# Performance work log

Measured on AMD Instinct MI355X. Metric: run time of the kernel, lower is better.

Reference implementation:

```python
import jax, jax.numpy as jnp
import numpy as np

N_USERS = 20000
N_ENTITIES = 80000
N = N_USERS + N_ENTITIES
EMBED_DIM = 128
CONV = [128, 128, 64, 32]  # [embed_dim] + eval(conv_dim_list)
NNZ = 1_600_000
CF_B = 8192
CF_L2_LAMBDA = 1e-5


def setup_inputs() -> dict:
    key = jax.random.key(0)
    ks = jax.random.split(key, 20)
    inp = {}
    inp["embed_table"] = jax.random.normal(ks[0], (N, EMBED_DIM), jnp.float32) * 0.02
    ki = 1
    for l in range(3):
        din, dout = CONV[l], CONV[l + 1]
        s = 1.0 / np.sqrt(din).astype(np.float32)
        inp[f"W1_{l}"] = jax.random.normal(ks[ki], (din, dout), jnp.float32) * s; ki += 1
        inp[f"b1_{l}"] = jnp.zeros((dout,), jnp.float32)
        inp[f"W2_{l}"] = jax.random.normal(ks[ki], (din, dout), jnp.float32) * s; ki += 1
        inp[f"b2_{l}"] = jnp.zeros((dout,), jnp.float32)
    inp["edge_rows"] = jax.random.randint(ks[7], (NNZ,), 0, N, jnp.int32)
    inp["edge_cols"] = jax.random.randint(ks[8], (NNZ,), 0, N, jnp.int32)
    # Laplacian-like normalized attention values (positive, ~1/degree scale)
    inp["edge_vals"] = jax.random.uniform(ks[9], (NNZ,), jnp.float32) / 16.0
    inp["user_ids"] = jax.random.randint(ks[10], (CF_B,), 0, N_USERS, jnp.int32)
    inp["item_pos_ids"] = jax.random.randint(ks[11], (CF_B,), N_USERS, N, jnp.int32)
    inp["item_neg_ids"] = jax.random.randint(ks[12], (CF_B,), N_USERS, N, jnp.int32)
    return inp


def _l2_normalize(x):
    # F.normalize(x, p=2, dim=1): x / max(||x||_2, eps)
    n = jnp.linalg.norm(x, axis=1, keepdims=True)
    return x / jnp.maximum(n, 1e-12)


def _l2_loss_mean(x):
    return jnp.mean(jnp.sum(x * x, axis=1) / 2.0)


def _calc_cf_embeddings(embed_table, layer_params, edge_rows, edge_cols, edge_vals):
    n = embed_table.shape[0]
    ego = embed_table
    outs = [ego]
    for (W1, b1, W2, b2) in layer_params:
        # sparse A @ ego via gather + segment_sum (SpMM in COO form)
        msgs = edge_vals[:, None] * ego[edge_cols]          # [nnz, d_in]
        side = jax.ops.segment_sum(msgs, edge_rows, num_segments=n)  # [n, d_in]
        # bi-interaction aggregator (mess_dropout = 0)
        ego = (jax.nn.leaky_relu((ego + side) @ W1 + b1)
               + jax.nn.leaky_relu((ego * side) @ W2 + b2))
        outs.append(_l2_normalize(ego))
    return jnp.concatenate(outs, axis=1)  # [n, 128+128+64+32]


def reference(embed_table, W1_0, b1_0, W2_0, b2_0, W1_1, b1_1, W2_1, b2_1,
              W1_2, b1_2, W2_2, b2_2, edge_rows, edge_cols, edge_vals,
              user_ids, item_pos_ids, item_neg_ids):
    layer_params = [(W1_0, b1_0, W2_0, b2_0),
                    (W1_1, b1_1, W2_1, b2_1),
                    (W1_2, b1_2, W2_2, b2_2)]
    all_embed = _calc_cf_embeddings(embed_table, layer_params,
                                    edge_rows, edge_cols, edge_vals)
    u = all_embed[user_ids]
    p = all_embed[item_pos_ids]
    ng = all_embed[item_neg_ids]
    pos_score = jnp.sum(u * p, axis=1)
    neg_score = jnp.sum(u * ng, axis=1)
    cf_loss = jnp.mean(-jax.nn.log_sigmoid(pos_score - neg_score))
    l2 = _l2_loss_mean(u) + _l2_loss_mean(p) + _l2_loss_mean(ng)
    return cf_loss + CF_L2_LAMBDA * l2
```

## Files before the change

### kernel.cpp

```cpp
#include <hip/hip_runtime.h>
#include <math.h>

static constexpr int N_NODES = 100000;
static constexpr int NNZ     = 1600000;
static constexpr int CFB     = 8192;
static constexpr int NBUCK   = (N_NODES + 63) / 64;
static constexpr int N4      = N_NODES * 128 / 4;
static constexpr int NCHUNK  = 128;
static constexpr int EPC     = NNZ / NCHUNK;
static constexpr int NE      = NBUCK * NCHUNK;
static constexpr int NBLK2   = (NE + 255) / 256;

typedef short bf16x8 __attribute__((ext_vector_type(8)));
typedef float f32x4  __attribute__((ext_vector_type(4)));

__device__ __forceinline__ float lrelu(float x) { return x >= 0.0f ? x : 0.01f * x; }

__device__ __forceinline__ unsigned short f2bf(float x) {
  unsigned u = __float_as_uint(x);
  u += 0x7FFFu + ((u >> 16) & 1u);
  return (unsigned short)(u >> 16);
}
__device__ __forceinline__ float bf2f(unsigned short h) {
  return __uint_as_float(((unsigned)h) << 16);
}
__device__ __forceinline__ unsigned pack2(float x, float y) {
  return (unsigned)f2bf(x) | ((unsigned)f2bf(y) << 16);
}

__global__ __launch_bounds__(256)
void cvt_bf16_kernel(const float* __restrict__ in, unsigned short* __restrict__ out) {
  int i = blockIdx.x * 256 + threadIdx.x;
  if (i < N4) {
    float4 v = reinterpret_cast<const float4*>(in)[i];
    uint2 o; o.x = pack2(v.x, v.y); o.y = pack2(v.z, v.w);
    reinterpret_cast<uint2*>(out)[i] = o;
  }
}

__global__ __launch_bounds__(256)
void binhist(const int* __restrict__ erows, int* __restrict__ cnt) {
  __shared__ int h[NBUCK];
  for (int b = threadIdx.x; b < NBUCK; b += 256) h[b] = 0;
  __syncthreads();
  const int c = blockIdx.x;
  const int e0 = c * EPC, e1 = e0 + EPC;
  for (int i = e0 + threadIdx.x; i < e1; i += 256)
    atomicAdd(&h[erows[i] >> 6], 1);
  __syncthreads();
  for (int b = threadIdx.x; b < NBUCK; b += 256)
    cnt[b * NCHUNK + c] = h[b];
}

__global__ __launch_bounds__(256)
void scan_reduce_g(const int* __restrict__ src, int* __restrict__ bsum, int n) {
  __shared__ int s[256];
  int i = blockIdx.x * 256 + threadIdx.x;
  s[threadIdx.x] = (i < n) ? src[i] : 0;
  __syncthreads();
  for (int st = 128; st > 0; st >>= 1) {
    if (threadIdx.x < st) s[threadIdx.x] += s[threadIdx.x + st];
    __syncthreads();
  }
  if (threadIdx.x == 0) bsum[blockIdx.x] = s[0];
}

__global__ __launch_bounds__(1024)
void scan_top_g(int* __restrict__ bsum, int nb) {
  __shared__ int s[1024];
  int t = threadIdx.x;
  int v0 = (t < nb) ? bsum[t] : 0;
  s[t] = v0;
  __syncthreads();
  for (int off = 1; off < 1024; off <<= 1) {
    int v = (t >= off) ? s[t - off] : 0;
    __syncthreads();
    s[t] += v;
    __syncthreads();
  }
  if (t < nb) bsum[t] = s[t] - v0;
}

__global__ __launch_bounds__(256)
void scan_final_g(int* __restrict__ data, const int* __restrict__ bsum, int n) {
  __shared__ int s[256];
  int t = threadIdx.x;
  int i = blockIdx.x * 256 + t;
  int v = (i < n) ? data[i] : 0;
  s[t] = v;
  __syncthreads();
  for (int off = 1; off < 256; off <<= 1) {
    int x = (t >= off) ? s[t - off] : 0;
    __syncthreads();
    s[t] += x;
    __syncthreads();
  }
  if (i < n) data[i] = s[t] - v + bsum[blockIdx.x];
}

__global__ __launch_bounds__(256)
void scatter_bucket(const int* __restrict__ erows, const int* __restrict__ ecols,
                    const float* __restrict__ evals, const int* __restrict__ off,
                    uint2* __restrict__ spackA) {
  __shared__ int cur[NBUCK];
  const int c = blockIdx.x;
  for (int b = threadIdx.x; b < NBUCK; b += 256)
    cur[b] = off[b * NCHUNK + c];
  __syncthreads();
  const int e0 = c * EPC, e1 = e0 + EPC;
  for (int i = e0 + threadIdx.x; i < e1; i += 256) {
    int r = erows[i];
    int p = atomicAdd(&cur[r >> 6], 1);
    uint2 rec;
    rec.x = (unsigned)ecols[i] | ((unsigned)(r & 63) << 17);
    rec.y = __float_as_uint(evals[i]);
    spackA[p] = rec;
  }
}

__global__ __launch_bounds__(256)
void bucket_sort(const int* __restrict__ off, const uint2* __restrict__ spackA,
                 uint2* __restrict__ spackB, int* __restrict__ row_ptr) {
  __shared__ int hist[64];
  __shared__ int hcur[64];
  const int b = blockIdx.x;
  const int tid = threadIdx.x;
  const int j0 = off[b * NCHUNK];
  const int j1 = (b + 1 < NBUCK) ? off[(b + 1) * NCHUNK] : NNZ;
  if (tid < 64) hist[tid] = 0;
  __syncthreads();
  for (int k = j0 + tid; k < j1; k += 256)
    atomicAdd(&hist[(spackA[k].x >> 17) & 63], 1);
  __syncthreads();
  if (tid == 0) {
    int s = 0, row0 = b * 64;
    for (int r = 0; r < 64; ++r) {
      int v = hist[r];
      hcur[r] = s;
      if (row0 + r < N_NODES) row_ptr[row0 + r] = j0 + s;
      s += v;
    }
    if (b == NBUCK - 1) row_ptr[N_NODES] = NNZ;
  }
  __syncthreads();
  for (int k = j0 + tid; k < j1; k += 256) {
    uint2 rec = spackA[k];
    int rl = (rec.x >> 17) & 63;
    int p = j0 + atomicAdd(&hcur[rl], 1);
    spackB[p] = rec;
  }
}

template<int DIN>
__global__ __launch_bounds__(256)
void spmm_csr(const unsigned short* __restrict__ ego,
              const int* __restrict__ row_ptr,
              const uint2* __restrict__ spack,
              unsigned short* __restrict__ side) {
  int row  = blockIdx.x * 4 + (threadIdx.x >> 6);
  int lane = threadIdx.x & 63;
  if (row >= N_NODES) return;
  int j0 = row_ptr[row], j1 = row_ptr[row + 1];
  if constexpr (DIN == 128) {
    float ax = 0.f, ay = 0.f;
    #pragma unroll 8
    for (int j = j0; j < j1; ++j) {
      uint2 rec = spack[j];
      float v = __uint_as_float(rec.y);
      unsigned x = *reinterpret_cast<const unsigned*>(ego + (size_t)(rec.x & 0x1FFFF) * 128 + lane * 2);
      ax += v * bf2f((unsigned short)(x & 0xFFFFu));
      ay += v * bf2f((unsigned short)(x >> 16));
    }
    *reinterpret_cast<unsigned*>(side + (size_t)row * 128 + lane * 2) = pack2(ax, ay);
  } else {
    float a = 0.f;
    #pragma unroll 8
    for (int j = j0; j < j1; ++j) {
      uint2 rec = spack[j];
      a += __uint_as_float(rec.y) * bf2f(ego[(size_t)(rec.x & 0x1FFFF) * DIN + lane]);
    }
    side[(size_t)row * DIN + lane] = f2bf(a);
  }
}

template<int DIN, int DOUT, int WM, int WN, int TPB>
__global__ __launch_bounds__(256)
void bi_mfma(const unsigned short* __restrict__ ego,
             const unsigned short* __restrict__ side,
             const float* __restrict__ W1, const float* __restrict__ b1,
             const float* __restrict__ W2, const float* __restrict__ b2,
             unsigned short* __restrict__ out) {
  static_assert(WM * WN == 4, "4 waves");
  constexpr int KFRAG = DIN / 32;
  constexpr int NCOLS = DOUT / WN;
  constexpr int NFRAG = NCOLS / 16;
  constexpr int MROWS = 32 / WM;
  constexpr int MFRAG = MROWS / 16;
  constexpr int CPR   = DIN / 8;
  constexpr int CHUNKS = 32 * CPR;

  __shared__ __align__(16) unsigned short lds1[32 * DIN];
  __shared__ __align__(16) unsigned short lds2[32 * DIN];

  const int tid  = threadIdx.x;
  const int wid  = tid >> 6;
  const int lane = tid & 63;
  const int n0   = (wid % WN) * NCOLS;
  const int mrow0 = (wid / WN) * MROWS;
  const int lr   = lane & 15;
  const int lk   = (lane >> 4) * 8;

  bf16x8 w1f[KFRAG][NFRAG], w2f[KFRAG][NFRAG];
  #pragma unroll
  for (int kf = 0; kf < KFRAG; ++kf)
    #pragma unroll
    for (int nf = 0; nf < NFRAG; ++nf) {
      int col = n0 + nf * 16 + lr;
      int kr  = kf * 32 + lk;
      bf16x8 a, b;
      #pragma unroll
      for (int j = 0; j < 8; ++j) {
        a[j] = (short)f2bf(W1[(size_t)(kr + j) * DOUT + col]);
        b[j] = (short)f2bf(W2[(size_t)(kr + j) * DOUT + col]);
      }
      w1f[kf][nf] = a; w2f[kf][nf] = b;
    }
  float b1v[NFRAG], b2v[NFRAG];
  #pragma unroll
  for (int nf = 0; nf < NFRAG; ++nf) {
    b1v[nf] = b1[n0 + nf * 16 + lr];
    b2v[nf] = b2[n0 + nf * 16 + lr];
  }

  for (int t = 0; t < TPB; ++t) {
    int row0 = (blockIdx.x * TPB + t) * 32;
    if (row0 >= N_NODES) break;
    __syncthreads();
    for (int ci = tid; ci < CHUNKS; ci += 256) {
      int r  = ci / CPR;
      int c8 = ci % CPR;
      size_t g = (size_t)(row0 + r) * DIN + c8 * 8;
      uint4 e4 = *reinterpret_cast<const uint4*>(ego + g);
      uint4 s4 = *reinterpret_cast<const uint4*>(side + g);
      uint4 h1v, h2v;
      {
        float ex, ey, sx, sy;
        ex = bf2f((unsigned short)(e4.x & 0xFFFFu)); ey = bf2f((unsigned short)(e4.x >> 16));
        sx = bf2f((unsigned short)(s4.x & 0xFFFFu)); sy = bf2f((unsigned short)(s4.x >> 16));
        h1v.x = pack2(ex + sx, ey + sy); h2v.x = pack2(ex * sx, ey * sy);
        ex = bf2f((unsigned short)(e4.y & 0xFFFFu)); ey = bf2f((unsigned short)(e4.y >> 16));
        sx = bf2f((unsigned short)(s4.y & 0xFFFFu)); sy = bf2f((unsigned short)(s4.y >> 16));
        h1v.y = pack2(ex + sx, ey + sy); h2v.y = pack2(ex * sx, ey * sy);
        ex = bf2f((unsigned short)(e4.z & 0xFFFFu)); ey = bf2f((unsigned short)(e4.z >> 16));
        sx = bf2f((unsigned short)(s4.z & 0xFFFFu)); sy = bf2f((unsigned short)(s4.z >> 16));
        h1v.z = pack2(ex + sx, ey + sy); h2v.z = pack2(ex * sx, ey * sy);
        ex = bf2f((unsigned short)(e4.w & 0xFFFFu)); ey = bf2f((unsigned short)(e4.w >> 16));
        sx = bf2f((unsigned short)(s4.w & 0xFFFFu)); sy = bf2f((unsigned short)(s4.w >> 16));
        h1v.w = pack2(ex + sx, ey + sy); h2v.w = pack2(ex * sx, ey * sy);
      }
      unsigned byte = ((unsigned)(r * DIN + c8 * 8)) * 2u;
      byte ^= (unsigned)((r & 7) << 4);
      *reinterpret_cast<uint4*>(reinterpret_cast<char*>(lds1) + byte) = h1v;
      *reinterpret_cast<uint4*>(reinterpret_cast<char*>(lds2) + byte) = h2v;
    }
    __syncthreads();

    f32x4 acc1[MFRAG][NFRAG], acc2[MFRAG][NFRAG];
    #pragma unroll
    for (int mf = 0; mf < MFRAG; ++mf)
      #pragma unroll
      for (int nf = 0; nf < NFRAG; ++nf) {
        acc1[mf][nf] = (f32x4)0.f;
        acc2[mf][nf] = (f32x4)0.f;
      }
    #pragma unroll
    for (int kf = 0; kf < KFRAG; ++kf) {
      bf16x8 a1[MFRAG], a2[MFRAG];
      #pragma unroll
      for (int mf = 0; mf < MFRAG; ++mf) {
        int r = mrow0 + mf * 16 + lr;
        unsigned byte = ((unsigned)(r * DIN + kf * 32 + lk)) * 2u;
        byte ^= (unsigned)((r & 7) << 4);
        a1[mf] = *reinterpret_cast<const bf16x8*>(reinterpret_cast<const char*>(lds1) + byte);
        a2[mf] = *reinterpret_cast<const bf16x8*>(reinterpret_cast<const char*>(lds2) + byte);
      }
      #pragma unroll
      for (int mf = 0; mf < MFRAG; ++mf)
        #pragma unroll
        for (int nf = 0; nf < NFRAG; ++nf) {
          acc1[mf][nf] = __builtin_amdgcn_mfma_f32_16x16x32_bf16(a1[mf], w1f[kf][nf], acc1[mf][nf], 0, 0, 0);
          acc2[mf][nf] = __builtin_amdgcn_mfma_f32_16x16x32_bf16(a2[mf], w2f[kf][nf], acc2[mf][nf], 0, 0, 0);
        }
    }

    #pragma unroll
    for (int mf = 0; mf < MFRAG; ++mf)
      #pragma unroll
      for (int nf = 0; nf < NFRAG; ++nf) {
        #pragma unroll
        for (int reg = 0; reg < 4; ++reg) {
          int r = row0 + mrow0 + mf * 16 + (lane >> 4) * 4 + reg;
          int c = n0 + nf * 16 + lr;
          float o = lrelu(acc1[mf][nf][reg] + b1v[nf]) + lrelu(acc2[mf][nf][reg] + b2v[nf]);
          out[(size_t)r * DOUT + c] = f2bf(o);
        }
      }
  }
}

__global__ __launch_bounds__(256)
void score_all(const float* __restrict__ emb0,
               const unsigned short* __restrict__ e1,
               const unsigned short* __restrict__ e2,
               const unsigned short* __restrict__ e3,
               const int* __restrict__ uid, const int* __restrict__ pid,
               const int* __restrict__ nid,
               float* __restrict__ pos, float* __restrict__ neg,
               float* __restrict__ l2) {
  int i = blockIdx.x * 4 + (threadIdx.x >> 6);
  int lane = threadIdx.x & 63;
  if (i >= CFB) return;
  const int ui = uid[i], pi = pid[i], gi = nid[i];
  float PS = 0.f, NS = 0.f, L2 = 0.f;

  {
    float up = 0, un = 0, uu = 0, pp = 0, nn = 0;
    for (int d = lane; d < 128; d += 64) {
      float a = emb0[(size_t)ui * 128 + d];
      float b = emb0[(size_t)pi * 128 + d];
      float c = emb0[(size_t)gi * 128 + d];
      up += a * b; un += a * c; uu += a * a; pp += b * b; nn += c * c;
    }
    #pragma unroll
    for (int off = 32; off > 0; off >>= 1) {
      up += __shfl_xor(up, off); un += __shfl_xor(un, off);
      uu += __shfl_xor(uu, off); pp += __shfl_xor(pp, off); nn += __shfl_xor(nn, off);
    }
    PS += up; NS += un; L2 += uu + pp + nn;
  }
  const unsigned short* tabs[3] = { e1, e2, e3 };
  const int dims[3] = { 128, 64, 32 };
  #pragma unroll
  for (int L = 0; L < 3; ++L) {
    const unsigned short* T = tabs[L];
    const int dim = dims[L];
    float up = 0, un = 0, uu = 0, pp = 0, nn = 0;
    for (int d = lane; d < dim; d += 64) {
      float a = bf2f(T[(size_t)ui * dim + d]);
      float b = bf2f(T[(size_t)pi * dim + d]);
      float c = bf2f(T[(size_t)gi * dim + d]);
      up += a * b; un += a * c; uu += a * a; pp += b * b; nn += c * c;
    }
    #pragma unroll
    for (int off = 32; off > 0; off >>= 1) {
      up += __shfl_xor(up, off); un += __shfl_xor(un, off);
      uu += __shfl_xor(uu, off); pp += __shfl_xor(pp, off); nn += __shfl_xor(nn, off);
    }
    float mu = fmaxf(sqrtf(uu), 1e-12f);
    float mp = fmaxf(sqrtf(pp), 1e-12f);
    float mn = fmaxf(sqrtf(nn), 1e-12f);
    PS += up / (mu * mp);
    NS += un / (mu * mn);
    L2 += uu / (mu * mu) + pp / (mp * mp) + nn / (mn * mn);
  }
  if (lane == 0) { pos[i] = PS; neg[i] = NS; l2[i] = L2; }
}

__global__ __launch_bounds__(256)
void loss_kernel(const float* __restrict__ pos, const float* __restrict__ neg,
                 const float* __restrict__ l2, float* __restrict__ out) {
  __shared__ float s1[256];
  __shared__ float s2[256];
  int tid = threadIdx.x;
  float cf = 0.f, reg = 0.f;
  for (int i = tid; i < CFB; i += 256) {
    float x = pos[i] - neg[i];
    float sp = (x > 0.f) ? log1pf(expf(-x)) : (-x + log1pf(expf(x)));
    cf  += sp;
    reg += l2[i];
  }
  s1[tid] = cf; s2[tid] = reg;
  __syncthreads();
  for (int s = 128; s > 0; s >>= 1) {
    if (tid < s) { s1[tid] += s1[tid + s]; s2[tid] += s2[tid + s]; }
    __syncthreads();
  }
  if (tid == 0)
    out[0] = s1[0] / (float)CFB + 1e-5f * (0.5f * s2[0] / (float)CFB);
}

extern "C" void kernel_launch(void* const* d_in, const int* in_sizes, int n_in,
                              void* d_out, int out_size, void* d_ws, size_t ws_size,
                              hipStream_t stream) {
  const float* embed = (const float*)d_in[0];
  const float* W1_0 = (const float*)d_in[1];
  const float* b1_0 = (const float*)d_in[2];
  const float* W2_0 = (const float*)d_in[3];
  const float* b2_0 = (const float*)d_in[4];
  const float* W1_1 = (const float*)d_in[5];
  const float* b1_1 = (const float*)d_in[6];
  const float* W2_1 = (const float*)d_in[7];
  const float* b2_1 = (const float*)d_in[8];
  const float* W1_2 = (const float*)d_in[9];
  const float* b1_2 = (const float*)d_in[10];
  const float* W2_2 = (const float*)d_in[11];
  const float* b2_2 = (const float*)d_in[12];
  const int*   erows = (const int*)d_in[13];
  const int*   ecols = (const int*)d_in[14];
  const float* evals = (const float*)d_in[15];
  const int*   uid = (const int*)d_in[16];
  const int*   pid = (const int*)d_in[17];
  const int*   nid = (const int*)d_in[18];

  unsigned short* e0 = (unsigned short*)d_ws;
  unsigned short* e1 = e0 + (size_t)N_NODES * 128;
  unsigned short* e2 = e1 + (size_t)N_NODES * 128;
  unsigned short* e3 = e2 + (size_t)N_NODES * 64;
  unsigned short* sb = e3 + (size_t)N_NODES * 32;
  int*   cnt     = (int*)(sb + (size_t)N_NODES * 128);
  int*   bsum    = cnt + NE;
  int*   row_ptr = bsum + 1024;
  uint2* spackA  = (uint2*)(row_ptr + N_NODES + 2);
  uint2* spackB  = spackA + NNZ;
  float* posb    = (float*)(spackB + NNZ);
  float* negb    = posb + CFB;
  float* l2b     = negb + CFB;

  cvt_bf16_kernel<<<(N4 + 255) / 256, 256, 0, stream>>>(embed, e0);
  binhist<<<NCHUNK, 256, 0, stream>>>(erows, cnt);
  scan_reduce_g<<<NBLK2, 256, 0, stream>>>(cnt, bsum, NE);
  scan_top_g<<<1, 1024, 0, stream>>>(bsum, NBLK2);
  scan_final_g<<<NBLK2, 256, 0, stream>>>(cnt, bsum, NE);
  scatter_bucket<<<NCHUNK, 256, 0, stream>>>(erows, ecols, evals, cnt, spackA);
  bucket_sort<<<NBUCK, 256, 0, stream>>>(cnt, spackA, spackB, row_ptr);

  constexpr int TPB = 5;
  constexpr int GB  = (N_NODES / 32 + TPB - 1) / TPB;

  spmm_csr<128><<<(N_NODES + 3) / 4, 256, 0, stream>>>(e0, row_ptr, spackB, sb);
  bi_mfma<128, 128, 1, 4, TPB><<<GB, 256, 0, stream>>>(e0, sb, W1_0, b1_0, W2_0, b2_0, e1);

  spmm_csr<128><<<(N_NODES + 3) / 4, 256, 0, stream>>>(e1, row_ptr, spackB, sb);
  bi_mfma<128, 64, 1, 4, TPB><<<GB, 256, 0, stream>>>(e1, sb, W1_1, b1_1, W2_1, b2_1, e2);

  spmm_csr<64><<<(N_NODES + 3) / 4, 256, 0, stream>>>(e2, row_ptr, spackB, sb);
  bi_mfma<64, 32, 2, 2, TPB><<<GB, 256, 0, stream>>>(e2, sb, W1_2, b1_2, W2_2, b2_2, e3);

  score_all<<<CFB / 4, 256, 0, stream>>>(embed, e1, e2, e3, uid, pid, nid, posb, negb, l2b);
  loss_kernel<<<1, 256, 0, stream>>>(posb, negb, l2b, (float*)d_out);
}
```

Before: 394.9 us.

## Gather SpMM neighbor features from scaled FP8 copies instead of BF16

Each layer's GEMM kernel and the initial conversion now also write an FP8 (e4m3) copy of the embeddings with a fixed per-layer scale. The SpMM gathers neighbor rows from these FP8 tables and rescales the accumulated sum, which halves the bytes fetched in the random-access gather. The cost is extra FP8 stores in the conversion and GEMM kernels, plus reduced precision with fixed scales that could saturate or underflow. The layer-1 FP8 table reuses the spackA scratch buffer after sorting has finished.

Result: no change. 390.6 us (-1.1%).

```diff
diff --git a/kernel.cpp b/kernel.cpp
--- a/kernel.cpp
+++ b/kernel.cpp
@@ -13,6 +13,7 @@
 
 typedef short bf16x8 __attribute__((ext_vector_type(8)));
 typedef float f32x4  __attribute__((ext_vector_type(4)));
+typedef float f32x2  __attribute__((ext_vector_type(2)));
 
 __device__ __forceinline__ float lrelu(float x) { return x >= 0.0f ? x : 0.01f * x; }
 
@@ -29,12 +30,16 @@
 }
 
 __global__ __launch_bounds__(256)
-void cvt_bf16_kernel(const float* __restrict__ in, unsigned short* __restrict__ out) {
+void cvt_kernel(const float* __restrict__ in, unsigned short* __restrict__ out_bf,
+                unsigned char* __restrict__ out_q) {
   int i = blockIdx.x * 256 + threadIdx.x;
   if (i < N4) {
     float4 v = reinterpret_cast<const float4*>(in)[i];
     uint2 o; o.x = pack2(v.x, v.y); o.y = pack2(v.z, v.w);
-    reinterpret_cast<uint2*>(out)[i] = o;
+    reinterpret_cast<uint2*>(out_bf)[i] = o;
+    int q = __builtin_amdgcn_cvt_pk_fp8_f32(v.x * 1024.f, v.y * 1024.f, 0, false);
+    q = __builtin_amdgcn_cvt_pk_fp8_f32(v.z * 1024.f, v.w * 1024.f, q, true);
+    reinterpret_cast<unsigned*>(out_q)[i] = (unsigned)q;
   }
 }
 
@@ -153,7 +158,7 @@
 
 template<int DIN>
 __global__ __launch_bounds__(256)
-void spmm_csr(const unsigned short* __restrict__ ego,
+void spmm_fp8(const unsigned char* __restrict__ qtab, float inv_scale,
               const int* __restrict__ row_ptr,
               const uint2* __restrict__ spack,
               unsigned short* __restrict__ side) {
@@ -167,29 +172,33 @@
     for (int j = j0; j < j1; ++j) {
       uint2 rec = spack[j];
       float v = __uint_as_float(rec.y);
-      unsigned x = *reinterpret_cast<const unsigned*>(ego + (size_t)(rec.x & 0x1FFFF) * 128 + lane * 2);
-      ax += v * bf2f((unsigned short)(x & 0xFFFFu));
-      ay += v * bf2f((unsigned short)(x >> 16));
-    }
-    *reinterpret_cast<unsigned*>(side + (size_t)row * 128 + lane * 2) = pack2(ax, ay);
+      unsigned q = *reinterpret_cast<const unsigned short*>(
+          qtab + (size_t)(rec.x & 0x1FFFF) * 128 + lane * 2);
+      f32x2 xy = __builtin_amdgcn_cvt_pk_f32_fp8(q, false);
+      ax += v * xy.x;  ay += v * xy.y;
+    }
+    *reinterpret_cast<unsigned*>(side + (size_t)row * 128 + lane * 2) =
+        pack2(ax * inv_scale, ay * inv_scale);
   } else {
     float a = 0.f;
     #pragma unroll 8
     for (int j = j0; j < j1; ++j) {
       uint2 rec = spack[j];
-      a += __uint_as_float(rec.y) * bf2f(ego[(size_t)(rec.x & 0x1FFFF) * DIN + lane]);
-    }
-    side[(size_t)row * DIN + lane] = f2bf(a);
-  }
-}
-
-template<int DIN, int DOUT, int WM, int WN, int TPB>
+      unsigned q = qtab[(size_t)(rec.x & 0x1FFFF) * DIN + lane];
+      a += __uint_as_float(rec.y) * __builtin_amdgcn_cvt_f32_fp8(q, 0);
+    }
+    side[(size_t)row * DIN + lane] = f2bf(a * inv_scale);
+  }
+}
+
+template<int DIN, int DOUT, int WM, int WN, int TPB, bool QOUT>
 __global__ __launch_bounds__(256)
 void bi_mfma(const unsigned short* __restrict__ ego,
              const unsigned short* __restrict__ side,
              const float* __restrict__ W1, const float* __restrict__ b1,
              const float* __restrict__ W2, const float* __restrict__ b2,
-             unsigned short* __restrict__ out) {
+             unsigned short* __restrict__ out,
+             unsigned char* __restrict__ outq, float qs) {
   static_assert(WM * WN == 4, "4 waves");
   constexpr int KFRAG = DIN / 32;
   constexpr int NCOLS = DOUT / WN;
@@ -303,6 +312,11 @@
           int c = n0 + nf * 16 + lr;
           float o = lrelu(acc1[mf][nf][reg] + b1v[nf]) + lrelu(acc2[mf][nf][reg] + b2v[nf]);
           out[(size_t)r * DOUT + c] = f2bf(o);
+          if constexpr (QOUT) {
+            float oq = o * qs;
+            outq[(size_t)r * DOUT + c] =
+                (unsigned char)(__builtin_amdgcn_cvt_pk_fp8_f32(oq, oq, 0, false) & 0xFF);
+          }
         }
       }
   }
@@ -417,16 +431,19 @@
   unsigned short* e2 = e1 + (size_t)N_NODES * 128;
   unsigned short* e3 = e2 + (size_t)N_NODES * 64;
   unsigned short* sb = e3 + (size_t)N_NODES * 32;
-  int*   cnt     = (int*)(sb + (size_t)N_NODES * 128);
+  unsigned char*  q0 = (unsigned char*)(sb + (size_t)N_NODES * 128);
+  unsigned char*  q2 = q0 + (size_t)N_NODES * 128;
+  int*   cnt     = (int*)(q2 + (size_t)N_NODES * 64);
   int*   bsum    = cnt + NE;
   int*   row_ptr = bsum + 1024;
   uint2* spackA  = (uint2*)(row_ptr + N_NODES + 2);
   uint2* spackB  = spackA + NNZ;
+  unsigned char* q1 = (unsigned char*)spackA;
   float* posb    = (float*)(spackB + NNZ);
   float* negb    = posb + CFB;
   float* l2b     = negb + CFB;
 
-  cvt_bf16_kernel<<<(N4 + 255) / 256, 256, 0, stream>>>(embed, e0);
+  cvt_kernel<<<(N4 + 255) / 256, 256, 0, stream>>>(embed, e0, q0);
   binhist<<<NCHUNK, 256, 0, stream>>>(erows, cnt);
   scan_reduce_g<<<NBLK2, 256, 0, stream>>>(cnt, bsum, NE);
   scan_top_g<<<1, 1024, 0, stream>>>(bsum, NBLK2);
@@ -437,14 +454,14 @@
   constexpr int TPB = 5;
   constexpr int GB  = (N_NODES / 32 + TPB - 1) / TPB;
 
-  spmm_csr<128><<<(N_NODES + 3) / 4, 256, 0, stream>>>(e0, row_ptr, spackB, sb);
-  bi_mfma<128, 128, 1, 4, TPB><<<GB, 256, 0, stream>>>(e0, sb, W1_0, b1_0, W2_0, b2_0, e1);
-
-  spmm_csr<128><<<(N_NODES + 3) / 4, 256, 0, stream>>>(e1, row_ptr, spackB, sb);
-  bi_mfma<128, 64, 1, 4, TPB><<<GB, 256, 0, stream>>>(e1, sb, W1_1, b1_1, W2_1, b2_1, e2);
-
-  spmm_csr<64><<<(N_NODES + 3) / 4, 256, 0, stream>>>(e2, row_ptr, spackB, sb);
-  bi_mfma<64, 32, 2, 2, TPB><<<GB, 256, 0, stream>>>(e2, sb, W1_2, b1_2, W2_2, b2_2, e3);
+  spmm_fp8<128><<<(N_NODES + 3) / 4, 256, 0, stream>>>(q0, 1.f / 1024.f, row_ptr, spackB, sb);
+  bi_mfma<128, 128, 1, 4, TPB, true><<<GB, 256, 0, stream>>>(e0, sb, W1_0, b1_0, W2_0, b2_0, e1, q1, 64.f);
+
+  spmm_fp8<128><<<(N_NODES + 3) / 4, 256, 0, stream>>>(q1, 1.f / 64.f, row_ptr, spackB, sb);
+  bi_mfma<128, 64, 1, 4, TPB, true><<<GB, 256, 0, stream>>>(e1, sb, W1_1, b1_1, W2_1, b2_1, e2, q2, 64.f);
+
+  spmm_fp8<64><<<(N_NODES + 3) / 4, 256, 0, stream>>>(q2, 1.f / 64.f, row_ptr, spackB, sb);
+  bi_mfma<64, 32, 2, 2, TPB, false><<<GB, 256, 0, stream>>>(e2, sb, W1_2, b1_2, W2_2, b2_2, e3, (unsigned char*)nullptr, 0.f);
 
   score_all<<<CFB / 4, 256, 0, stream>>>(embed, e1, e2, e3, uid, pid, nid, posb, negb, l2b);
   loss_kernel<<<1, 256, 0, stream>>>(posb, negb, l2b, (float*)d_out);
```
